# Optimization experiments

Hardware: AMD Instinct MI355X
Metric: run time of the kernel (lower is better)

Reference implementation:

```python
import jax, jax.numpy as jnp
import numpy as np

HIDDEN = 4096
N_HEADS = 8
HEAD = HIDDEN // N_HEADS  # 512
SCALE = float(HIDDEN) ** 0.5  # NOTE: module MULTIPLIES by sqrt(hidden_dim), faithful to source
NEG = -1e9


def setup_inputs() -> dict:
    key = jax.random.key(0)
    ks = jax.random.split(key, 7)
    B, S = 4, 2048
    q = jax.random.normal(ks[0], (B, S, HIDDEN), dtype=jnp.float32)
    k = jax.random.normal(ks[1], (B, S, HIDDEN), dtype=jnp.float32)
    v = jax.random.normal(ks[2], (B, S, HIDDEN), dtype=jnp.float32)
    mask = jax.random.randint(ks[3], (B, S), 0, 2, dtype=jnp.int32)
    w_std = 1.0 / np.sqrt(HIDDEN)
    Wq = jax.random.normal(ks[4], (HEAD, HIDDEN), dtype=jnp.float32) * w_std
    Wk = jax.random.normal(ks[5], (HEAD, HIDDEN), dtype=jnp.float32) * w_std
    Wv = jax.random.normal(ks[6], (HEAD, HIDDEN), dtype=jnp.float32) * w_std
    return {"q": q, "k": k, "v": v, "mask": mask, "Wq": Wq, "Wk": Wk, "Wv": Wv}


def reference(q, k, v, mask, Wq, Wk, Wv):
    # bias-free linear projections (nn.Linear: x @ W.T)
    qh = jnp.einsum('bse,de->bsd', q, Wq)  # [B,S,HEAD]
    kh = jnp.einsum('bse,de->bsd', k, Wk)
    vh = jnp.einsum('bse,de->bsd', v, Wv)
    # scores: q @ k^T, then MULTIPLY by sqrt(hidden_dim) as in source
    scores = jnp.einsum('bsd,btd->bst', qh, kh) * SCALE  # [B,S,S]
    # additive mask over keys: mask [B,S] -> [B,1,S]; done under no_grad in torch
    scores = jnp.where(mask[:, None, :] == 0, NEG, scores)
    scores = jax.lax.stop_gradient(scores)  # torch no_grad reassignment detaches
    attn = jax.nn.softmax(scores, axis=-1)
    # dropout p=0.0 -> identity
    out = jnp.einsum('bst,btd->bsd', attn, vh)  # [B,S,HEAD]
    return out
```

## Files before the change

kernel.cpp:

```cpp
#include <hip/hip_runtime.h>

#define HIDDEN 4096
#define HEADD  512
#define SEQ    2048
#define NBATCH 4
#define KSPLIT 4
#define KRANGE (SEQ/KSPLIT)
#define KSTR   520

typedef float f32x4 __attribute__((ext_vector_type(4)));
typedef short s16x8 __attribute__((ext_vector_type(8)));

__device__ __forceinline__ unsigned short f2bf(float x){
  unsigned u = __float_as_uint(x);
  u += 0x7fffu + ((u >> 16) & 1u);
  return (unsigned short)(u >> 16);
}
__device__ __forceinline__ float bf2f(unsigned short b){
  return __uint_as_float(((unsigned)b) << 16);
}
__device__ __forceinline__ void gl_lds16(const unsigned short* g, unsigned short* l){
  __builtin_amdgcn_global_load_lds((const __attribute__((address_space(1))) unsigned int*)g,
                                   (__attribute__((address_space(3))) unsigned int*)l,
                                   16, 0, 0);
}


__global__ void wsplit_kernel(const float* __restrict__ Wq,
                              const float* __restrict__ Wk,
                              const float* __restrict__ Wv,
                              unsigned short* __restrict__ wqh, unsigned short* __restrict__ wql,
                              unsigned short* __restrict__ wkh, unsigned short* __restrict__ wkl,
                              unsigned short* __restrict__ wvh){
  const int n4 = HEADD * HIDDEN / 4;
  for (int i = blockIdx.x * blockDim.x + threadIdx.x; i < n4; i += gridDim.x * blockDim.x){
    float4 a = ((const float4*)Wq)[i];
    ushort4 h, lo;
    h.x = f2bf(a.x); lo.x = f2bf(a.x - bf2f(h.x));
    h.y = f2bf(a.y); lo.y = f2bf(a.y - bf2f(h.y));
    h.z = f2bf(a.z); lo.z = f2bf(a.z - bf2f(h.z));
    h.w = f2bf(a.w); lo.w = f2bf(a.w - bf2f(h.w));
    ((ushort4*)wqh)[i] = h; ((ushort4*)wql)[i] = lo;
    a = ((const float4*)Wk)[i];
    h.x = f2bf(a.x); lo.x = f2bf(a.x - bf2f(h.x));
    h.y = f2bf(a.y); lo.y = f2bf(a.y - bf2f(h.y));
    h.z = f2bf(a.z); lo.z = f2bf(a.z - bf2f(h.z));
    h.w = f2bf(a.w); lo.w = f2bf(a.w - bf2f(h.w));
    ((ushort4*)wkh)[i] = h; ((ushort4*)wkl)[i] = lo;
    a = ((const float4*)Wv)[i];
    h.x = f2bf(a.x); h.y = f2bf(a.y); h.z = f2bf(a.z); h.w = f2bf(a.w);
    ((ushort4*)wvh)[i] = h;
  }
}

template<int SPLITS, int MODE>
__global__ __launch_bounds__(512, 4)
void proj_kernel(const float* __restrict__ X,
                 const unsigned short* __restrict__ Wh,
                 const unsigned short* __restrict__ Wl,
                 unsigned short* __restrict__ Ohi,
                 unsigned short* __restrict__ Olo,
                 unsigned short* __restrict__ OvT){
  __shared__ unsigned short Ah[2][128*32];
  __shared__ unsigned short Al[(SPLITS>=3)?2*128*32:8];
  __shared__ unsigned short Bh[2][128*32];
  __shared__ unsigned short Bl[(SPLITS>=3)?2*128*32:8];

  const int tid  = threadIdx.x;
  const int lane = tid & 63, wid = tid >> 6;
  const int quad = lane >> 4, l16 = lane & 15;
  const int wm = wid >> 1, wn = wid & 1;
  const int m0 = blockIdx.y * 128, n0 = blockIdx.x * 128;

  const int sB    = (lane & 7) ^ (lane >> 3);
  const int browS = ((lane >> 3) << 1) + (sB >> 2);
  const int bcolS = (sB & 3) << 3;

  const int fbase = ((l16 >> 1) << 6) + ((((((l16 & 1) << 2) | quad)) ^ (l16 >> 1)) << 3);

  f32x4 acc[2][4];
  #pragma unroll
  for (int i = 0; i < 2; i++)
    #pragma unroll
    for (int j = 0; j < 4; j++){
      f32x4 z = {0.f, 0.f, 0.f, 0.f};
      acc[i][j] = z;
    }

  float4 xa[4];
  int ar[4], ahalf[4], acin[4], aidx[4];
  #pragma unroll
  for (int c = 0; c < 4; c++){
    int chunk = tid + c * 512;
    ar[c]    = chunk >> 4;
    int col4 = (chunk & 15) << 2;
    ahalf[c] = col4 >> 5;
    acin[c]  = col4 & 31;
    int R  = ar[c] >> 1;
    int sA = (((ar[c] & 1) << 2) | (acin[c] >> 3)) ^ (R & 7);
    aidx[c] = (R << 6) + (sA << 3) + (acin[c] & 7);
    xa[c] = *(const float4*)(X + (size_t)(m0 + ar[c]) * HIDDEN + col4);
  }

  for (int k0 = 0; k0 < HIDDEN; k0 += 64){
    #pragma unroll
    for (int c = 0; c < 4; c++){
      ushort4 hv;
      hv.x = f2bf(xa[c].x); hv.y = f2bf(xa[c].y); hv.z = f2bf(xa[c].z); hv.w = f2bf(xa[c].w);
      *(ushort4*)(&Ah[ahalf[c]][aidx[c]]) = hv;
      if (SPLITS >= 3){
        ushort4 lv;
        lv.x = f2bf(xa[c].x - bf2f(hv.x));
        lv.y = f2bf(xa[c].y - bf2f(hv.y));
        lv.z = f2bf(xa[c].z - bf2f(hv.z));
        lv.w = f2bf(xa[c].w - bf2f(hv.w));
        *(ushort4*)(&Al[ahalf[c]*4096 + aidx[c]]) = lv;
      }
    }
    #pragma unroll
    for (int h = 0; h < 2; h++){
      const unsigned short* gh = Wh + (size_t)(n0 + wid*16 + browS) * HIDDEN + k0 + h*32 + bcolS;
      gl_lds16(gh, &Bh[h][wid*512]);
      if (SPLITS >= 3){
        const unsigned short* gl = Wl + (size_t)(n0 + wid*16 + browS) * HIDDEN + k0 + h*32 + bcolS;
        gl_lds16(gl, &Bl[h*4096 + wid*512]);
      }
    }
    __syncthreads();
    if (k0 + 64 < HIDDEN){
      #pragma unroll
      for (int c = 0; c < 4; c++){
        int col4 = ahalf[c]*32 + acin[c];
        xa[c] = *(const float4*)(X + (size_t)(m0 + ar[c]) * HIDDEN + k0 + 64 + col4);
      }
    }
    #pragma unroll
    for (int h = 0; h < 2; h++){
      s16x8 ah[2], al[2], bh[4], bl[4];
      #pragma unroll
      for (int i = 0; i < 2; i++){
        ah[i] = *(const s16x8*)(&Ah[h][(wm*32 + i*16)*32 + fbase]);
        if (SPLITS >= 3) al[i] = *(const s16x8*)(&Al[h*4096 + (wm*32 + i*16)*32 + fbase]);
      }
      #pragma unroll
      for (int j = 0; j < 4; j++){
        bh[j] = *(const s16x8*)(&Bh[h][(wn*64 + j*16)*32 + fbase]);
        if (SPLITS >= 3) bl[j] = *(const s16x8*)(&Bl[h*4096 + (wn*64 + j*16)*32 + fbase]);
      }
      #pragma unroll
      for (int i = 0; i < 2; i++)
        #pragma unroll
        for (int j = 0; j < 4; j++){
          acc[i][j] = __builtin_amdgcn_mfma_f32_16x16x32_bf16(ah[i], bh[j], acc[i][j], 0, 0, 0);
          if (SPLITS >= 3){
            acc[i][j] = __builtin_amdgcn_mfma_f32_16x16x32_bf16(ah[i], bl[j], acc[i][j], 0, 0, 0);
            acc[i][j] = __builtin_amdgcn_mfma_f32_16x16x32_bf16(al[i], bh[j], acc[i][j], 0, 0, 0);
          }
        }
    }
    __syncthreads();
  }

  if (MODE == 0){
    #pragma unroll
    for (int i = 0; i < 2; i++)
      #pragma unroll
      for (int j = 0; j < 4; j++)
        #pragma unroll
        for (int r = 0; r < 4; r++){
          int m = m0 + wm*32 + i*16 + quad*4 + r;
          int n = n0 + wn*64 + j*16 + l16;
          float c = acc[i][j][r];
          unsigned short h = f2bf(c);
          Ohi[(size_t)m * HEADD + n] = h;
          Olo[(size_t)m * HEADD + n] = f2bf(c - bf2f(h));
        }
  } else {
    #pragma unroll
    for (int i = 0; i < 2; i++)
      #pragma unroll
      for (int j = 0; j < 4; j++){
        int mbase = m0 + wm*32 + i*16 + quad*4;
        int d = n0 + wn*64 + j*16 + l16;
        int b = mbase >> 11;
        int t = mbase & 2047;
        ushort4 vv;
        vv.x = f2bf(acc[i][j][0]);
        vv.y = f2bf(acc[i][j][1]);
        vv.z = f2bf(acc[i][j][2]);
        vv.w = f2bf(acc[i][j][3]);
        *(ushort4*)(OvT + ((size_t)(b * HEADD + d)) * SEQ + t) = vv;
      }
  }
}

__global__ __launch_bounds__(512, 2)
void flash_kernel(const unsigned short* __restrict__ qhh, const unsigned short* __restrict__ qhl,
                  const unsigned short* __restrict__ khh, const unsigned short* __restrict__ khl,
                  const unsigned short* __restrict__ vhT, const int* __restrict__ mask,
                  float* __restrict__ part, float* __restrict__ ml){
  __shared__ unsigned short Kh[32*KSTR];
  __shared__ unsigned short Kl[32*KSTR];
  __shared__ unsigned short Vt[512*32];
  __shared__ unsigned short Pt[8*512];

  const int tid = threadIdx.x, lane = tid & 63, wid = tid >> 6;
  const int quad = lane >> 4, l16 = lane & 15;

  const int wg  = blockIdx.x + (int)gridDim.x * (blockIdx.y + (int)gridDim.y * blockIdx.z);
  const int lwg = (wg & 7) * 32 + (wg >> 3);
  const int qt = lwg & 15;
  const int kz = (lwg >> 4) & 3;
  const int b  = lwg >> 6;
  const int qrow0 = qt * 128 + wid * 16;
  const int kbase = kz * KRANGE;

  const int sV   = (lane & 7) ^ (lane >> 3);
  const int vdro = ((lane >> 3) << 1) + (sV >> 2);
  const int vcol = (sV & 3) << 3;
  const int vbase = ((l16 >> 1) << 6) + ((((((l16 & 1) << 2) | quad)) ^ (l16 >> 1)) << 3);

  const size_t qoff = ((size_t)(b * SEQ) + qrow0 + l16) * HEADD + quad * 8;
  s16x8 qh[16];
  #pragma unroll
  for (int ds = 0; ds < 16; ds++) qh[ds] = *(const s16x8*)(qhh + qoff + ds*32);

  float mrow[4], lrow[4];
  #pragma unroll
  for (int r = 0; r < 4; r++){ mrow[r] = -3.0e38f; lrow[r] = 0.f; }
  f32x4 oacc[32];
  #pragma unroll
  for (int j = 0; j < 32; j++){
    f32x4 z = {0.f, 0.f, 0.f, 0.f};
    oacc[j] = z;
  }

  auto stageK = [&](int kt){
    #pragma unroll
    for (int c = 0; c < 4; c++){
      int keyl = wid*4 + c;
      size_t g = ((size_t)(b * SEQ) + kbase + kt + keyl) * HEADD + lane*8;
      gl_lds16(khh + g, Kh + keyl*KSTR);
      gl_lds16(khl + g, Kl + keyl*KSTR);
    }
  };
  auto stageV = [&](int kt){
    #pragma unroll
    for (int c = 0; c < 4; c++){
      int d0 = wid*64 + c*16;
      const unsigned short* vs = vhT + ((size_t)(b * HEADD) + d0 + vdro) * SEQ
                                     + kbase + kt + vcol;
      gl_lds16(vs, Vt + d0*32);
    }
  };

  stageK(0);
  stageV(0);
  __syncthreads();

  for (int kt = 0; kt < KRANGE; kt += 32){
    const bool has_next = (kt + 32 < KRANGE);
    const int key0 = kbase + kt + l16;
    const int mk0 = mask[b * SEQ + key0];
    const int mk1 = mask[b * SEQ + key0 + 16];

    f32x4 s0 = {0.f,0.f,0.f,0.f}, s1 = {0.f,0.f,0.f,0.f};
    #pragma unroll
    for (int ds = 0; ds < 16; ds++){
      s16x8 aL  = *(const s16x8*)(qhl + qoff + ds*32);
      s16x8 b0H = *(const s16x8*)(Kh + l16*KSTR      + ds*32 + quad*8);
      s16x8 b0L = *(const s16x8*)(Kl + l16*KSTR      + ds*32 + quad*8);
      s16x8 b1H = *(const s16x8*)(Kh + (16+l16)*KSTR + ds*32 + quad*8);
      s16x8 b1L = *(const s16x8*)(Kl + (16+l16)*KSTR + ds*32 + quad*8);
      s0 = __builtin_amdgcn_mfma_f32_16x16x32_bf16(qh[ds], b0H, s0, 0, 0, 0);
      s0 = __builtin_amdgcn_mfma_f32_16x16x32_bf16(qh[ds], b0L, s0, 0, 0, 0);
      s0 = __builtin_amdgcn_mfma_f32_16x16x32_bf16(aL,     b0H, s0, 0, 0, 0);
      s0 = __builtin_amdgcn_mfma_f32_16x16x32_bf16(aL,     b0L, s0, 0, 0, 0);
      s1 = __builtin_amdgcn_mfma_f32_16x16x32_bf16(qh[ds], b1H, s1, 0, 0, 0);
      s1 = __builtin_amdgcn_mfma_f32_16x16x32_bf16(qh[ds], b1L, s1, 0, 0, 0);
      s1 = __builtin_amdgcn_mfma_f32_16x16x32_bf16(aL,     b1H, s1, 0, 0, 0);
      s1 = __builtin_amdgcn_mfma_f32_16x16x32_bf16(aL,     b1L, s1, 0, 0, 0);
    }

    __syncthreads();

    if (has_next) stageK(kt + 32);

    float sm0[4], sm1[4];
    #pragma unroll
    for (int r = 0; r < 4; r++){
      sm0[r] = mk0 ? s0[r] * 64.0f : -1.0e9f;
      sm1[r] = mk1 ? s1[r] * 64.0f : -1.0e9f;
    }
    float rm[4];
    #pragma unroll
    for (int r = 0; r < 4; r++) rm[r] = fmaxf(sm0[r], sm1[r]);
    #pragma unroll
    for (int sh = 1; sh < 16; sh <<= 1){
      #pragma unroll
      for (int r = 0; r < 4; r++) rm[r] = fmaxf(rm[r], __shfl_xor(rm[r], sh, 64));
    }
    float alpha[4], p0[4], p1[4], rs[4];
    #pragma unroll
    for (int r = 0; r < 4; r++){
      float mn = fmaxf(mrow[r], rm[r]);
      alpha[r] = __expf(mrow[r] - mn);
      mrow[r] = mn;
      p0[r] = __expf(sm0[r] - mn);
      p1[r] = __expf(sm1[r] - mn);
      rs[r] = p0[r] + p1[r];
    }
    #pragma unroll
    for (int sh = 1; sh < 16; sh <<= 1){
      #pragma unroll
      for (int r = 0; r < 4; r++) rs[r] += __shfl_xor(rs[r], sh, 64);
    }
    #pragma unroll
    for (int r = 0; r < 4; r++) lrow[r] = lrow[r] * alpha[r] + rs[r];
    #pragma unroll
    for (int r = 0; r < 4; r++){
      Pt[wid*512 + (quad*4 + r)*32 + l16]      = f2bf(p0[r]);
      Pt[wid*512 + (quad*4 + r)*32 + 16 + l16] = f2bf(p1[r]);
    }
    #pragma unroll
    for (int j = 0; j < 32; j++)
      #pragma unroll
      for (int r = 0; r < 4; r++) oacc[j][r] *= alpha[r];
    s16x8 pa = *(const s16x8*)(Pt + wid*512 + l16*32 + quad*8);
    #pragma unroll
    for (int j = 0; j < 32; j++){
      s16x8 vb = *(const s16x8*)(Vt + j*512 + vbase);
      oacc[j] = __builtin_amdgcn_mfma_f32_16x16x32_bf16(pa, vb, oacc[j], 0, 0, 0);
    }

    __syncthreads();

    if (has_next) stageV(kt + 32);
  }

  const size_t prow = (size_t)(kz * (NBATCH*SEQ)) + b * SEQ + qrow0;
  #pragma unroll
  for (int j = 0; j < 32; j++)
    #pragma unroll
    for (int r = 0; r < 4; r++)
      part[(prow + quad*4 + r) * HEADD + j*16 + l16] = oacc[j][r];
  if (l16 == 0){
    #pragma unroll
    for (int r = 0; r < 4; r++){
      ml[(prow + quad*4 + r)*2 + 0] = mrow[r];
      ml[(prow + quad*4 + r)*2 + 1] = lrow[r];
    }
  }
}

__global__ __launch_bounds__(256)
void reduce_kernel(const float* __restrict__ part, const float* __restrict__ ml,
                   float* __restrict__ out){
  const int row = blockIdx.x;
  const int t = threadIdx.x;
  float m[KSPLIT], l[KSPLIT];
  float M = -3.0e38f;
  #pragma unroll
  for (int j = 0; j < KSPLIT; j++){
    m[j] = ml[((size_t)j*(NBATCH*SEQ) + row)*2 + 0];
    l[j] = ml[((size_t)j*(NBATCH*SEQ) + row)*2 + 1];
    M = fmaxf(M, m[j]);
  }
  float w[KSPLIT], L = 0.f;
  #pragma unroll
  for (int j = 0; j < KSPLIT; j++){
    w[j] = __expf(m[j] - M);
    L += w[j] * l[j];
  }
  const float invL = 1.0f / L;
  #pragma unroll
  for (int c = 0; c < 2; c++){
    int d = t + c*256;
    float acc = 0.f;
    #pragma unroll
    for (int j = 0; j < KSPLIT; j++)
      acc += w[j] * part[((size_t)j*(NBATCH*SEQ) + row)*HEADD + d];
    out[(size_t)row * HEADD + d] = acc * invL;
  }
}

extern "C" void kernel_launch(void* const* d_in, const int* in_sizes, int n_in,
                              void* d_out, int out_size, void* d_ws, size_t ws_size,
                              hipStream_t stream){
  const float* q    = (const float*)d_in[0];
  const float* k    = (const float*)d_in[1];
  const float* v    = (const float*)d_in[2];
  const int*   mask = (const int*)d_in[3];
  const float* Wq   = (const float*)d_in[4];
  const float* Wk   = (const float*)d_in[5];
  const float* Wv   = (const float*)d_in[6];
  float* out = (float*)d_out;

  char* ws = (char*)d_ws;
  const size_t MB = 1024 * 1024;
  unsigned short* wqh = (unsigned short*)(ws + 0*MB);
  unsigned short* wql = (unsigned short*)(ws + 4*MB);
  unsigned short* wkh = (unsigned short*)(ws + 8*MB);
  unsigned short* wkl = (unsigned short*)(ws + 12*MB);
  unsigned short* wvh = (unsigned short*)(ws + 16*MB);
  unsigned short* qhh = (unsigned short*)(ws + 20*MB);
  unsigned short* qhl = (unsigned short*)(ws + 28*MB);
  unsigned short* khh = (unsigned short*)(ws + 36*MB);
  unsigned short* khl = (unsigned short*)(ws + 44*MB);
  unsigned short* vhT = (unsigned short*)(ws + 52*MB);
  float*          part = (float*)(ws + 60*MB);
  float*          mlb  = (float*)(ws + 124*MB);

  hipLaunchKernelGGL(wsplit_kernel, dim3(1024), dim3(256), 0, stream,
                     Wq, Wk, Wv, wqh, wql, wkh, wkl, wvh);
  hipLaunchKernelGGL((proj_kernel<3,0>), dim3(4, 64), dim3(512), 0, stream,
                     q, wqh, wql, qhh, qhl, (unsigned short*)nullptr);
  hipLaunchKernelGGL((proj_kernel<3,0>), dim3(4, 64), dim3(512), 0, stream,
                     k, wkh, wkl, khh, khl, (unsigned short*)nullptr);
  hipLaunchKernelGGL((proj_kernel<1,1>), dim3(4, 64), dim3(512), 0, stream,
                     v, wvh, wvh, (unsigned short*)nullptr, (unsigned short*)nullptr, vhT);
  hipLaunchKernelGGL(flash_kernel, dim3(SEQ/128, KSPLIT, NBATCH), dim3(512), 0, stream,
                     qhh, qhl, khh, khl, vhT, mask, part, mlb);
  hipLaunchKernelGGL(reduce_kernel, dim3(NBATCH*SEQ), dim3(256), 0, stream,
                     part, mlb, out);
}
```

Baseline: 920.4 us.

## Merge Q/K/V projections into one launch and add lazy softmax rescaling

The three projection launches become a single kernel over a 3-deep grid. Block IDs are remapped so work interleaves across XCDs, and Q/K versus V behaviour is chosen at runtime from a flag instead of template parameters. This aims to fill the GPU better (768 blocks in one launch instead of three launches of 256) and cut launch gaps. The V path now gets a shared-memory footprint sized for the full split and carries runtime branches. Separately, the flash kernel skips the running-max update and the accumulator rescale unless the new row max exceeds the old one by more than 10, using a wave vote. This saves exp calls and 128 multiplies per step, while the softmax stays exact because the max cancels out.

Measured after the change: 839.2 us. 8.8% less time.

```diff
diff --git a/kernel.cpp b/kernel.cpp
--- a/kernel.cpp
+++ b/kernel.cpp
@@ -24,7 +24,6 @@
                                    (__attribute__((address_space(3))) unsigned int*)l,
                                    16, 0, 0);
 }
-
 
 __global__ void wsplit_kernel(const float* __restrict__ Wq,
                               const float* __restrict__ Wk,
@@ -53,24 +52,37 @@
   }
 }
 
-template<int SPLITS, int MODE>
 __global__ __launch_bounds__(512, 4)
-void proj_kernel(const float* __restrict__ X,
-                 const unsigned short* __restrict__ Wh,
-                 const unsigned short* __restrict__ Wl,
-                 unsigned short* __restrict__ Ohi,
-                 unsigned short* __restrict__ Olo,
-                 unsigned short* __restrict__ OvT){
+void proj_all_kernel(const float* __restrict__ q, const float* __restrict__ k,
+                     const float* __restrict__ v,
+                     const unsigned short* __restrict__ wqh, const unsigned short* __restrict__ wql,
+                     const unsigned short* __restrict__ wkh, const unsigned short* __restrict__ wkl,
+                     const unsigned short* __restrict__ wvh,
+                     unsigned short* __restrict__ qhh, unsigned short* __restrict__ qhl,
+                     unsigned short* __restrict__ khh, unsigned short* __restrict__ khl,
+                     unsigned short* __restrict__ vhT){
   __shared__ unsigned short Ah[2][128*32];
-  __shared__ unsigned short Al[(SPLITS>=3)?2*128*32:8];
+  __shared__ unsigned short Al[2*128*32];
   __shared__ unsigned short Bh[2][128*32];
-  __shared__ unsigned short Bl[(SPLITS>=3)?2*128*32:8];
+  __shared__ unsigned short Bl[2*128*32];
 
   const int tid  = threadIdx.x;
   const int lane = tid & 63, wid = tid >> 6;
   const int quad = lane >> 4, l16 = lane & 15;
   const int wm = wid >> 1, wn = wid & 1;
-  const int m0 = blockIdx.y * 128, n0 = blockIdx.x * 128;
+
+  const int wg  = blockIdx.x + 4 * blockIdx.y + 256 * blockIdx.z;
+  const int lwg = (wg & 7) * 96 + (wg >> 3);
+  const int n0 = (lwg & 3) * 128;
+  const int m0 = ((lwg >> 2) & 63) * 128;
+  const int z  = lwg >> 8;
+
+  const float* X = (z == 0) ? q : (z == 1) ? k : v;
+  const unsigned short* Wh = (z == 0) ? wqh : (z == 1) ? wkh : wvh;
+  const unsigned short* Wl = (z == 0) ? wql : (z == 1) ? wkl : wvh;
+  unsigned short* Ohi = (z == 0) ? qhh : khh;
+  unsigned short* Olo = (z == 0) ? qhl : khl;
+  const bool full = (z < 2);
 
   const int sB    = (lane & 7) ^ (lane >> 3);
   const int browS = ((lane >> 3) << 1) + (sB >> 2);
@@ -83,8 +95,8 @@
   for (int i = 0; i < 2; i++)
     #pragma unroll
     for (int j = 0; j < 4; j++){
-      f32x4 z = {0.f, 0.f, 0.f, 0.f};
-      acc[i][j] = z;
+      f32x4 zz = {0.f, 0.f, 0.f, 0.f};
+      acc[i][j] = zz;
     }
 
   float4 xa[4];
@@ -108,7 +120,7 @@
       ushort4 hv;
       hv.x = f2bf(xa[c].x); hv.y = f2bf(xa[c].y); hv.z = f2bf(xa[c].z); hv.w = f2bf(xa[c].w);
       *(ushort4*)(&Ah[ahalf[c]][aidx[c]]) = hv;
-      if (SPLITS >= 3){
+      if (full){
         ushort4 lv;
         lv.x = f2bf(xa[c].x - bf2f(hv.x));
         lv.y = f2bf(xa[c].y - bf2f(hv.y));
@@ -121,7 +133,7 @@
     for (int h = 0; h < 2; h++){
       const unsigned short* gh = Wh + (size_t)(n0 + wid*16 + browS) * HIDDEN + k0 + h*32 + bcolS;
       gl_lds16(gh, &Bh[h][wid*512]);
-      if (SPLITS >= 3){
+      if (full){
         const unsigned short* gl = Wl + (size_t)(n0 + wid*16 + browS) * HIDDEN + k0 + h*32 + bcolS;
         gl_lds16(gl, &Bl[h*4096 + wid*512]);
       }
@@ -140,19 +152,19 @@
       #pragma unroll
       for (int i = 0; i < 2; i++){
         ah[i] = *(const s16x8*)(&Ah[h][(wm*32 + i*16)*32 + fbase]);
-        if (SPLITS >= 3) al[i] = *(const s16x8*)(&Al[h*4096 + (wm*32 + i*16)*32 + fbase]);
+        if (full) al[i] = *(const s16x8*)(&Al[h*4096 + (wm*32 + i*16)*32 + fbase]);
       }
       #pragma unroll
       for (int j = 0; j < 4; j++){
         bh[j] = *(const s16x8*)(&Bh[h][(wn*64 + j*16)*32 + fbase]);
-        if (SPLITS >= 3) bl[j] = *(const s16x8*)(&Bl[h*4096 + (wn*64 + j*16)*32 + fbase]);
+        if (full) bl[j] = *(const s16x8*)(&Bl[h*4096 + (wn*64 + j*16)*32 + fbase]);
       }
       #pragma unroll
       for (int i = 0; i < 2; i++)
         #pragma unroll
         for (int j = 0; j < 4; j++){
           acc[i][j] = __builtin_amdgcn_mfma_f32_16x16x32_bf16(ah[i], bh[j], acc[i][j], 0, 0, 0);
-          if (SPLITS >= 3){
+          if (full){
             acc[i][j] = __builtin_amdgcn_mfma_f32_16x16x32_bf16(ah[i], bl[j], acc[i][j], 0, 0, 0);
             acc[i][j] = __builtin_amdgcn_mfma_f32_16x16x32_bf16(al[i], bh[j], acc[i][j], 0, 0, 0);
           }
@@ -161,7 +173,7 @@
     __syncthreads();
   }
 
-  if (MODE == 0){
+  if (full){
     #pragma unroll
     for (int i = 0; i < 2; i++)
       #pragma unroll
@@ -189,7 +201,7 @@
         vv.y = f2bf(acc[i][j][1]);
         vv.z = f2bf(acc[i][j][2]);
         vv.w = f2bf(acc[i][j][3]);
-        *(ushort4*)(OvT + ((size_t)(b * HEADD + d)) * SEQ + t) = vv;
+        *(ushort4*)(vhT + ((size_t)(b * HEADD + d)) * SEQ + t) = vv;
       }
   }
 }
@@ -300,14 +312,27 @@
       #pragma unroll
       for (int r = 0; r < 4; r++) rm[r] = fmaxf(rm[r], __shfl_xor(rm[r], sh, 64));
     }
-    float alpha[4], p0[4], p1[4], rs[4];
+    bool needv = false;
+    #pragma unroll
+    for (int r = 0; r < 4; r++) needv = needv || (rm[r] > mrow[r] + 10.0f);
+    const bool dorescale = (__any(needv ? 1 : 0) != 0);
+    float alpha[4];
+    if (dorescale){
+      #pragma unroll
+      for (int r = 0; r < 4; r++){
+        float mn = fmaxf(mrow[r], rm[r]);
+        alpha[r] = __expf(mrow[r] - mn);
+        mrow[r] = mn;
+      }
+    } else {
+      #pragma unroll
+      for (int r = 0; r < 4; r++) alpha[r] = 1.0f;
+    }
+    float p0[4], p1[4], rs[4];
     #pragma unroll
     for (int r = 0; r < 4; r++){
-      float mn = fmaxf(mrow[r], rm[r]);
-      alpha[r] = __expf(mrow[r] - mn);
-      mrow[r] = mn;
-      p0[r] = __expf(sm0[r] - mn);
-      p1[r] = __expf(sm1[r] - mn);
+      p0[r] = __expf(sm0[r] - mrow[r]);
+      p1[r] = __expf(sm1[r] - mrow[r]);
       rs[r] = p0[r] + p1[r];
     }
     #pragma unroll
@@ -322,10 +347,12 @@
       Pt[wid*512 + (quad*4 + r)*32 + l16]      = f2bf(p0[r]);
       Pt[wid*512 + (quad*4 + r)*32 + 16 + l16] = f2bf(p1[r]);
     }
-    #pragma unroll
-    for (int j = 0; j < 32; j++)
-      #pragma unroll
-      for (int r = 0; r < 4; r++) oacc[j][r] *= alpha[r];
+    if (dorescale){
+      #pragma unroll
+      for (int j = 0; j < 32; j++)
+        #pragma unroll
+        for (int r = 0; r < 4; r++) oacc[j][r] *= alpha[r];
+    }
     s16x8 pa = *(const s16x8*)(Pt + wid*512 + l16*32 + quad*8);
     #pragma unroll
     for (int j = 0; j < 32; j++){
@@ -413,12 +440,8 @@
 
   hipLaunchKernelGGL(wsplit_kernel, dim3(1024), dim3(256), 0, stream,
                      Wq, Wk, Wv, wqh, wql, wkh, wkl, wvh);
-  hipLaunchKernelGGL((proj_kernel<3,0>), dim3(4, 64), dim3(512), 0, stream,
-                     q, wqh, wql, qhh, qhl, (unsigned short*)nullptr);
-  hipLaunchKernelGGL((proj_kernel<3,0>), dim3(4, 64), dim3(512), 0, stream,
-                     k, wkh, wkl, khh, khl, (unsigned short*)nullptr);
-  hipLaunchKernelGGL((proj_kernel<1,1>), dim3(4, 64), dim3(512), 0, stream,
-                     v, wvh, wvh, (unsigned short*)nullptr, (unsigned short*)nullptr, vhT);
+  hipLaunchKernelGGL(proj_all_kernel, dim3(4, 64, 3), dim3(512), 0, stream,
+                     q, k, v, wqh, wql, wkh, wkl, wvh, qhh, qhl, khh, khl, vhT);
   hipLaunchKernelGGL(flash_kernel, dim3(SEQ/128, KSPLIT, NBATCH), dim3(512), 0, stream,
                      qhh, qhl, khh, khl, vhT, mask, part, mlb);
   hipLaunchKernelGGL(reduce_kernel, dim3(NBATCH*SEQ), dim3(256), 0, stream,
```
